# Kernel optimization log

Measured on AMD Instinct MI355X. Metric: run time of the kernel, lower is better.

Reference implementation:

```python
import jax, jax.numpy as jnp
import numpy as np

# class -> task group (from class_groups), and per-class distance thresholds
GROUP = jnp.array([0, 1, 1, 2, 2, 3, 4, 4, 5, 5], dtype=jnp.int32)
HIGH_T = jnp.array([2.0, 2.5, 2.5, 3.5, 2.5, 0.5, 1.0, 1.0, 0.5, 0.5], dtype=jnp.float32)
MED_T = jnp.array([4.0, 4.0, 4.0, 4.0, 4.0, 2.5, 2.5, 2.5, 2.0, 2.0], dtype=jnp.float32)
NEAR_THRESH = 30.0
FAR_THRESH = 50.0
FP_THRESH = 4.0


def setup_inputs() -> dict:
    key = jax.random.key(0)
    ks = jax.random.split(key, 7)
    B, R, G = 8, 4096, 512
    roi_xy = jax.random.uniform(ks[0], (B, R, 2), minval=-54.0, maxval=54.0)
    roi_rest = jax.random.normal(ks[1], (B, R, 7))
    rois = jnp.concatenate([roi_xy, roi_rest], axis=-1)            # (B,R,9)
    roi_scores = jax.random.uniform(ks[2], (B, R))                  # (B,R)
    roi_labels = jax.random.randint(ks[3], (B, R), 0, 10)           # (B,R)
    gt_xy = jax.random.uniform(ks[4], (B, G, 2), minval=-54.0, maxval=54.0)
    gt_rest = jax.random.normal(ks[5], (B, G, 7))
    gt_cls = jax.random.randint(ks[6], (B, G), 0, 10).astype(jnp.float32)
    gt_boxes_and_cls = jnp.concatenate([gt_xy, gt_rest, gt_cls[..., None]], axis=-1)  # (B,G,10)
    return {"rois": rois, "roi_scores": roi_scores, "gt_boxes_and_cls": gt_boxes_and_cls,
            "roi_labels": roi_labels, "batch_size": B}


def _forward(rois, roi_scores, gt, roi_labels):
    B, R, _ = rois.shape
    G = gt.shape[1]
    f32 = rois.dtype
    valid_roi = rois.sum(-1) != 0                                   # (B,R) padding filter
    valid_gt = gt.sum(-1) != 0                                      # (B,G)
    gt_cls = jnp.clip(gt[..., -1].astype(jnp.int32), 0, 9)         # (B,G)
    roi_grp = GROUP[jnp.clip(roi_labels.astype(jnp.int32), 0, 9)]  # (B,R)
    gt_grp = GROUP[gt_cls]                                          # (B,G)

    # BEV center distances (B,R,G) using x,y only
    diff = rois[:, :, None, :2] - gt[:, None, :, :2]
    d = jnp.sqrt((diff ** 2).sum(-1))

    same = roi_grp[:, :, None] == gt_grp[:, None, :]
    pv = valid_roi[:, :, None] & valid_gt[:, None, :]
    ht = HIGH_T[gt_cls][:, None, :]                                 # (B,1,G)->bcast
    mt = MED_T[gt_cls][:, None, :]
    high_mask = (d <= ht) & same & pv                               # (B,R,G)
    med_mask = (d > ht) & (d <= mt) & same & pv

    NEG = jnp.asarray(-1e9, f32)
    has_high = high_mask.any(axis=1)                                # (B,G)
    has_med = med_mask.any(axis=1)

    # best-scoring high ROI per GT
    hi = jnp.argmax(jnp.where(high_mask, roi_scores[:, :, None], NEG), axis=1)  # (B,G)
    high_roi = jnp.take_along_axis(rois, hi[:, :, None], axis=1)    # (B,G,9)
    high_score = jnp.take_along_axis(roi_scores, hi, axis=1)        # (B,G)
    refined_score = jnp.minimum((1.2 + high_score) / 2.0, 1.0)

    # best-scoring medium ROI per GT (used only when no high match)
    mi = jnp.argmax(jnp.where(med_mask, roi_scores[:, :, None], NEG), axis=1)
    med_roi = jnp.take_along_axis(rois, mi[:, :, None], axis=1)
    med_score = jnp.take_along_axis(roi_scores, mi, axis=1)
    sel_med = (~has_high) & has_med

    # unmatched GTs bucketed by range from ego (near/medium/far)
    unmatched = valid_gt & (~has_high) & (~has_med)
    rng = jnp.sqrt(gt[..., 0] ** 2 + gt[..., 1] ** 2)
    near = unmatched & (rng < NEAR_THRESH)
    far = unmatched & (rng > FAR_THRESH)
    midb = unmatched & (~near) & (~far)

    # false-positive ROIs: min distance to any valid GT > 4.0
    dmin = jnp.min(jnp.where(valid_gt[:, None, :], d, jnp.inf), axis=2)  # (B,R)
    fp = valid_roi & (dmin > FP_THRESH)

    hv = has_high.astype(f32)[..., None]
    mv = sel_med.astype(f32)[..., None]
    matched = (has_high | sel_med).astype(f32)[..., None]
    onehot = jnp.stack([near, midb, far], axis=-1).astype(f32)      # (B,G,3)
    outG = jnp.concatenate([
        high_roi * hv, (refined_score[..., None]) * hv, hv,
        med_roi * mv, (med_score[..., None]) * mv, mv,
        gt * matched, onehot], axis=-1)                             # (B,G,35)
    fpf = fp.astype(f32)
    outR = jnp.stack([fpf * roi_scores, fpf], axis=-1)              # (B,R,2)
    return jnp.concatenate([outG.reshape(B, -1), outR.reshape(B, -1)], axis=1)


def reference(rois, roi_scores, gt_boxes_and_cls, roi_labels, batch_size):
    return _forward(rois, roi_scores, gt_boxes_and_cls, roi_labels)
```

## Files before the change

### kernel.cpp

```cpp
#include <hip/hip_runtime.h>
#include <stdint.h>

#define NB 8
#define NR 4096
#define NG 512
#define OUTG 35
#define PER_B (NG*OUTG + NR*2)
#define GT_BLOCKS 512
#define FP_BLOCKS 128

__constant__ int   c_GROUP[10] = {0,1,1,2,2,3,4,4,5,5};
__constant__ float c_HIGH[10]  = {2.0f,2.5f,2.5f,3.5f,2.5f,0.5f,1.0f,1.0f,0.5f,0.5f};
__constant__ float c_MED[10]   = {4.0f,4.0f,4.0f,4.0f,4.0f,2.5f,2.5f,2.5f,2.0f,2.0f};

__device__ __forceinline__ float sqrt_le_bound(float t) {
  float B = t * t;
  while (sqrtf(__uint_as_float(__float_as_uint(B) + 1u)) <= t)
    B = __uint_as_float(__float_as_uint(B) + 1u);
  return B;
}

__global__ __launch_bounds__(256) void prep_kernel(
    const float* __restrict__ rois,
    const float* __restrict__ scores,
    const float* __restrict__ gt,
    const int*   __restrict__ labels,
    float4* __restrict__ ws_roi,
    float4* __restrict__ ws_gt) {
  int tid = blockIdx.x * 256 + threadIdx.x;
  if (tid < NB * NR) {
    const float* rr = rois + (size_t)tid * 9;
    float s = rr[0];
    #pragma unroll
    for (int k = 1; k < 9; ++k) s += rr[k];
    bool valid = (s != 0.0f);
    int lab = labels[tid];
    lab = min(max(lab, 0), 9);
    float w = valid ? (float)c_GROUP[lab] : -1.0f;
    ws_roi[tid] = make_float4(rr[0], rr[1], scores[tid], w);
  } else if (tid < NB * NR + NB * NG) {
    int i = tid - NB * NR;
    const float* gr = gt + (size_t)i * 10;
    float s = gr[0];
    #pragma unroll
    for (int k = 1; k < 10; ++k) s += gr[k];
    bool valid = (s != 0.0f);
    ws_gt[i] = make_float4(valid ? gr[0] : 1e30f, valid ? gr[1] : 1e30f, 0.f, 0.f);
  }
}

__device__ __forceinline__ void write_gt_row(
    float* __restrict__ og, const float gv[10], bool gvalid,
    unsigned long long uh, unsigned long long um,
    const float* __restrict__ rois_b) {
  bool has_high = (uh != 0ull);
  bool has_med  = (um != 0ull);
  bool sel_med  = (!has_high) && has_med;
  bool matched  = has_high || has_med;
  int   hi  = NR - 1 - (int)(unsigned int)(uh & 0xffffffffull);
  int   mi  = NR - 1 - (int)(unsigned int)(um & 0xffffffffull);
  float hsc = __uint_as_float((unsigned int)(uh >> 32) - 1u);
  float msc = __uint_as_float((unsigned int)(um >> 32) - 1u);
  const float* hr = rois_b + (size_t)(has_high ? hi : 0) * 9;
  const float* mr = rois_b + (size_t)(sel_med ? mi : 0) * 9;
  #pragma unroll
  for (int k = 0; k < 9; ++k) og[k] = has_high ? hr[k] : 0.0f;
  og[9]  = has_high ? fminf((1.2f + hsc) * 0.5f, 1.0f) : 0.0f;
  og[10] = has_high ? 1.0f : 0.0f;
  #pragma unroll
  for (int k = 0; k < 9; ++k) og[11 + k] = sel_med ? mr[k] : 0.0f;
  og[20] = sel_med ? msc : 0.0f;
  og[21] = sel_med ? 1.0f : 0.0f;
  #pragma unroll
  for (int k = 0; k < 10; ++k) og[22 + k] = matched ? gv[k] : 0.0f;
  bool unmatched = gvalid && !has_high && !has_med;
  float rng  = sqrtf(__fmul_rn(gv[0], gv[0]) + __fmul_rn(gv[1], gv[1]));
  bool nearb = unmatched && (rng < 30.0f);
  bool farb  = unmatched && (rng > 50.0f);
  bool midb  = unmatched && !nearb && !farb;
  og[32] = nearb ? 1.0f : 0.0f;
  og[33] = midb  ? 1.0f : 0.0f;
  og[34] = farb  ? 1.0f : 0.0f;
}

__global__ __launch_bounds__(256) void main_kernel(
    const float* __restrict__ rois,
    const float* __restrict__ gt,
    const float4* __restrict__ ws_roi,
    const float4* __restrict__ ws_gt,
    float* __restrict__ out) {
  __shared__ float2 sgt[NG];

  if (blockIdx.x < GT_BLOCKS) {
    int wave = threadIdx.x >> 6;
    int lane = threadIdx.x & 63;
    int widx = blockIdx.x * 4 + wave;
    int idx0 = widx * 2;
    int b    = idx0 >> 9;

    float gv0[10], gv1[10];
    {
      const float* g0 = gt + (size_t)idx0 * 10;
      #pragma unroll
      for (int k = 0; k < 10; ++k) gv0[k] = g0[k];
      #pragma unroll
      for (int k = 0; k < 10; ++k) gv1[k] = g0[10 + k];
    }
    float s0 = gv0[0], s1 = gv1[0];
    #pragma unroll
    for (int k = 1; k < 10; ++k) { s0 += gv0[k]; s1 += gv1[k]; }
    bool gvalid0 = (s0 != 0.0f), gvalid1 = (s1 != 0.0f);

    int cls0 = min(max((int)gv0[9], 0), 9);
    int cls1 = min(max((int)gv1[9], 0), 9);
    float Bh0 = sqrt_le_bound(c_HIGH[cls0]);
    float Bm0 = sqrt_le_bound(c_MED[cls0]);
    float Bh1 = sqrt_le_bound(c_HIGH[cls1]);
    float Bm1 = sqrt_le_bound(c_MED[cls1]);
    float gw0 = gvalid0 ? (float)c_GROUP[cls0] : -2.0f;
    float gw1 = gvalid1 ? (float)c_GROUP[cls1] : -2.0f;
    float gx0 = gv0[0], gy0 = gv0[1];
    float gx1 = gv1[0], gy1 = gv1[1];

    const float4* rp = ws_roi + (size_t)b * NR;
    unsigned long long uh0 = 0ull, um0 = 0ull, uh1 = 0ull, um1 = 0ull;
    #pragma unroll 4
    for (int r = lane; r < NR; r += 64) {
      float4 p = rp[r];
      unsigned long long key =
          ((unsigned long long)(__float_as_uint(p.z) + 1u) << 32) |
          (unsigned int)(NR - 1 - r);
      {
        float dx = p.x - gx0, dy = p.y - gy0;
        float d2 = __fmul_rn(dx, dx) + __fmul_rn(dy, dy);
        bool mm = (p.w == gw0) && (d2 <= Bm0);
        bool hh = mm && (d2 <= Bh0);
        bool ee = mm && !(d2 <= Bh0);
        if (hh && key > uh0) uh0 = key;
        if (ee && key > um0) um0 = key;
      }
      {
        float dx = p.x - gx1, dy = p.y - gy1;
        float d2 = __fmul_rn(dx, dx) + __fmul_rn(dy, dy);
        bool mm = (p.w == gw1) && (d2 <= Bm1);
        bool hh = mm && (d2 <= Bh1);
        bool ee = mm && !(d2 <= Bh1);
        if (hh && key > uh1) uh1 = key;
        if (ee && key > um1) um1 = key;
      }
    }
    #pragma unroll
    for (int off = 32; off > 0; off >>= 1) {
      unsigned long long t;
      t = __shfl_xor(uh0, off, 64); if (t > uh0) uh0 = t;
      t = __shfl_xor(um0, off, 64); if (t > um0) um0 = t;
      t = __shfl_xor(uh1, off, 64); if (t > uh1) uh1 = t;
      t = __shfl_xor(um1, off, 64); if (t > um1) um1 = t;
    }

    const float* rois_b = rois + (size_t)b * NR * 9;
    float* outb = out + (size_t)b * PER_B;
    if (lane == 0) {
      write_gt_row(outb + (size_t)(idx0 & 511) * OUTG, gv0, gvalid0, uh0, um0, rois_b);
    } else if (lane == 1) {
      write_gt_row(outb + (size_t)((idx0 + 1) & 511) * OUTG, gv1, gvalid1, uh1, um1, rois_b);
    }
  } else {
    int fb = blockIdx.x - GT_BLOCKS;
    int b  = fb >> 4;
    int r  = ((fb & 15) << 8) + threadIdx.x;

    const float4* gp = ws_gt + (size_t)b * NG;
    for (int j = threadIdx.x; j < NG; j += 256) {
      float4 v = gp[j];
      sgt[j] = make_float2(v.x, v.y);
    }
    __syncthreads();

    float4 p = ws_roi[(size_t)b * NR + r];
    float m2 = __builtin_inff();
    #pragma unroll 8
    for (int j = 0; j < NG; ++j) {
      float2 q = sgt[j];
      float dx = p.x - q.x, dy = p.y - q.y;
      float d2 = __fmul_rn(dx, dx) + __fmul_rn(dy, dy);
      m2 = fminf(m2, d2);
    }
    bool fp = (p.w >= 0.0f) && (sqrtf(m2) > 4.0f);
    float* orow = out + (size_t)b * PER_B + NG * OUTG + (size_t)r * 2;
    orow[0] = fp ? p.z : 0.0f;
    orow[1] = fp ? 1.0f : 0.0f;
  }
}

extern "C" void kernel_launch(void* const* d_in, const int* in_sizes, int n_in,
                              void* d_out, int out_size, void* d_ws, size_t ws_size,
                              hipStream_t stream) {
  const float* rois   = (const float*)d_in[0];
  const float* scores = (const float*)d_in[1];
  const float* gt     = (const float*)d_in[2];
  const int*   labels = (const int*)d_in[3];
  float* out = (float*)d_out;

  float4* ws_roi = (float4*)d_ws;
  float4* ws_gt  = ws_roi + (size_t)NB * NR;

  int total = NB * NR + NB * NG;
  prep_kernel<<<(total + 255) / 256, 256, 0, stream>>>(rois, scores, gt, labels,
                                                       ws_roi, ws_gt);
  main_kernel<<<GT_BLOCKS + FP_BLOCKS, 256, 0, stream>>>(rois, gt, ws_roi, ws_gt, out);
}
```

Before: 97.06 us.

## Fuse prep and main kernels, staging per-batch ROIs in shared memory

Removes the separate prep kernel and its workspace round trip. Each of 256 blocks (512 threads) now recomputes the packed ROI and GT records for its whole batch into shared memory (64KB of float4 plus 4KB), then does both the GT matching scan and a slice of the false-positive min-distance search. The FP search is split four ways per ROI with a shuffle reduction. This saves a launch and global traffic, at the cost of redundant per-batch prep work repeated 32 times per batch and lower occupancy from the large shared footprint.

```diff
diff --git a/kernel.cpp b/kernel.cpp
--- a/kernel.cpp
+++ b/kernel.cpp
@@ -6,8 +6,6 @@
 #define NG 512
 #define OUTG 35
 #define PER_B (NG*OUTG + NR*2)
-#define GT_BLOCKS 512
-#define FP_BLOCKS 128
 
 __constant__ int   c_GROUP[10] = {0,1,1,2,2,3,4,4,5,5};
 __constant__ float c_HIGH[10]  = {2.0f,2.5f,2.5f,3.5f,2.5f,0.5f,1.0f,1.0f,0.5f,0.5f};
@@ -18,35 +16,6 @@
   while (sqrtf(__uint_as_float(__float_as_uint(B) + 1u)) <= t)
     B = __uint_as_float(__float_as_uint(B) + 1u);
   return B;
-}
-
-__global__ __launch_bounds__(256) void prep_kernel(
-    const float* __restrict__ rois,
-    const float* __restrict__ scores,
-    const float* __restrict__ gt,
-    const int*   __restrict__ labels,
-    float4* __restrict__ ws_roi,
-    float4* __restrict__ ws_gt) {
-  int tid = blockIdx.x * 256 + threadIdx.x;
-  if (tid < NB * NR) {
-    const float* rr = rois + (size_t)tid * 9;
-    float s = rr[0];
-    #pragma unroll
-    for (int k = 1; k < 9; ++k) s += rr[k];
-    bool valid = (s != 0.0f);
-    int lab = labels[tid];
-    lab = min(max(lab, 0), 9);
-    float w = valid ? (float)c_GROUP[lab] : -1.0f;
-    ws_roi[tid] = make_float4(rr[0], rr[1], scores[tid], w);
-  } else if (tid < NB * NR + NB * NG) {
-    int i = tid - NB * NR;
-    const float* gr = gt + (size_t)i * 10;
-    float s = gr[0];
-    #pragma unroll
-    for (int k = 1; k < 10; ++k) s += gr[k];
-    bool valid = (s != 0.0f);
-    ws_gt[i] = make_float4(valid ? gr[0] : 1e30f, valid ? gr[1] : 1e30f, 0.f, 0.f);
-  }
 }
 
 __device__ __forceinline__ void write_gt_row(
@@ -83,113 +52,140 @@
   og[34] = farb  ? 1.0f : 0.0f;
 }
 
-__global__ __launch_bounds__(256) void main_kernel(
+__global__ __launch_bounds__(512) void fused_kernel(
     const float* __restrict__ rois,
+    const float* __restrict__ scores,
     const float* __restrict__ gt,
-    const float4* __restrict__ ws_roi,
-    const float4* __restrict__ ws_gt,
+    const int*   __restrict__ labels,
     float* __restrict__ out) {
+  __shared__ float4 sroi[NR];
   __shared__ float2 sgt[NG];
 
-  if (blockIdx.x < GT_BLOCKS) {
-    int wave = threadIdx.x >> 6;
-    int lane = threadIdx.x & 63;
-    int widx = blockIdx.x * 4 + wave;
-    int idx0 = widx * 2;
-    int b    = idx0 >> 9;
-
-    float gv0[10], gv1[10];
+  int tid = threadIdx.x;
+  int bid = blockIdx.x;
+  int b   = bid >> 5;
+  int sub = bid & 31;
+
+  const float* rois_b = rois   + (size_t)b * NR * 9;
+  const float* sc_b   = scores + (size_t)b * NR;
+  const int*   lab_b  = labels + (size_t)b * NR;
+  const float* gt_b   = gt     + (size_t)b * NG * 10;
+
+  #pragma unroll 4
+  for (int k = 0; k < 8; ++k) {
+    int r = tid + k * 512;
+    const float* rr = rois_b + (size_t)r * 9;
+    float s = rr[0];
+    #pragma unroll
+    for (int j = 1; j < 9; ++j) s += rr[j];
+    bool valid = (s != 0.0f);
+    int lab = min(max(lab_b[r], 0), 9);
+    float w = valid ? (float)c_GROUP[lab] : -1.0f;
+    sroi[r] = make_float4(rr[0], rr[1], sc_b[r], w);
+  }
+  {
+    const float* gr = gt_b + (size_t)tid * 10;
+    float s = gr[0];
+    #pragma unroll
+    for (int j = 1; j < 10; ++j) s += gr[j];
+    bool valid = (s != 0.0f);
+    sgt[tid] = make_float2(valid ? gr[0] : 1e30f, valid ? gr[1] : 1e30f);
+  }
+  __syncthreads();
+
+  int wave = tid >> 6;
+  int lane = tid & 63;
+  int g0   = sub * 16 + wave * 2;
+
+  float gv0[10], gv1[10];
+  {
+    const float* gp = gt_b + (size_t)g0 * 10;
+    #pragma unroll
+    for (int k = 0; k < 10; ++k) gv0[k] = gp[k];
+    #pragma unroll
+    for (int k = 0; k < 10; ++k) gv1[k] = gp[10 + k];
+  }
+  float s0 = gv0[0], s1 = gv1[0];
+  #pragma unroll
+  for (int k = 1; k < 10; ++k) { s0 += gv0[k]; s1 += gv1[k]; }
+  bool gvalid0 = (s0 != 0.0f), gvalid1 = (s1 != 0.0f);
+
+  int cls0 = min(max((int)gv0[9], 0), 9);
+  int cls1 = min(max((int)gv1[9], 0), 9);
+  float Bh0 = sqrt_le_bound(c_HIGH[cls0]);
+  float Bm0 = sqrt_le_bound(c_MED[cls0]);
+  float Bh1 = sqrt_le_bound(c_HIGH[cls1]);
+  float Bm1 = sqrt_le_bound(c_MED[cls1]);
+  float gw0 = gvalid0 ? (float)c_GROUP[cls0] : -2.0f;
+  float gw1 = gvalid1 ? (float)c_GROUP[cls1] : -2.0f;
+  float gx0 = gv0[0], gy0 = gv0[1];
+  float gx1 = gv1[0], gy1 = gv1[1];
+
+  unsigned long long uh0 = 0ull, um0 = 0ull, uh1 = 0ull, um1 = 0ull;
+  #pragma unroll 4
+  for (int r = lane; r < NR; r += 64) {
+    float4 p = sroi[r];
+    unsigned long long key =
+        ((unsigned long long)(__float_as_uint(p.z) + 1u) << 32) |
+        (unsigned int)(NR - 1 - r);
     {
-      const float* g0 = gt + (size_t)idx0 * 10;
-      #pragma unroll
-      for (int k = 0; k < 10; ++k) gv0[k] = g0[k];
-      #pragma unroll
-      for (int k = 0; k < 10; ++k) gv1[k] = g0[10 + k];
-    }
-    float s0 = gv0[0], s1 = gv1[0];
-    #pragma unroll
-    for (int k = 1; k < 10; ++k) { s0 += gv0[k]; s1 += gv1[k]; }
-    bool gvalid0 = (s0 != 0.0f), gvalid1 = (s1 != 0.0f);
-
-    int cls0 = min(max((int)gv0[9], 0), 9);
-    int cls1 = min(max((int)gv1[9], 0), 9);
-    float Bh0 = sqrt_le_bound(c_HIGH[cls0]);
-    float Bm0 = sqrt_le_bound(c_MED[cls0]);
-    float Bh1 = sqrt_le_bound(c_HIGH[cls1]);
-    float Bm1 = sqrt_le_bound(c_MED[cls1]);
-    float gw0 = gvalid0 ? (float)c_GROUP[cls0] : -2.0f;
-    float gw1 = gvalid1 ? (float)c_GROUP[cls1] : -2.0f;
-    float gx0 = gv0[0], gy0 = gv0[1];
-    float gx1 = gv1[0], gy1 = gv1[1];
-
-    const float4* rp = ws_roi + (size_t)b * NR;
-    unsigned long long uh0 = 0ull, um0 = 0ull, uh1 = 0ull, um1 = 0ull;
+      float dx = p.x - gx0, dy = p.y - gy0;
+      float d2 = __fmul_rn(dx, dx) + __fmul_rn(dy, dy);
+      bool mm = (p.w == gw0) && (d2 <= Bm0);
+      bool hh = mm && (d2 <= Bh0);
+      bool ee = mm && !(d2 <= Bh0);
+      if (hh && key > uh0) uh0 = key;
+      if (ee && key > um0) um0 = key;
+    }
+    {
+      float dx = p.x - gx1, dy = p.y - gy1;
+      float d2 = __fmul_rn(dx, dx) + __fmul_rn(dy, dy);
+      bool mm = (p.w == gw1) && (d2 <= Bm1);
+      bool hh = mm && (d2 <= Bh1);
+      bool ee = mm && !(d2 <= Bh1);
+      if (hh && key > uh1) uh1 = key;
+      if (ee && key > um1) um1 = key;
+    }
+  }
+  #pragma unroll
+  for (int off = 32; off > 0; off >>= 1) {
+    unsigned long long t;
+    t = __shfl_xor(uh0, off, 64); if (t > uh0) uh0 = t;
+    t = __shfl_xor(um0, off, 64); if (t > um0) um0 = t;
+    t = __shfl_xor(uh1, off, 64); if (t > uh1) uh1 = t;
+    t = __shfl_xor(um1, off, 64); if (t > um1) um1 = t;
+  }
+
+  float* outb = out + (size_t)b * PER_B;
+  if (lane == 0) {
+    write_gt_row(outb + (size_t)g0 * OUTG, gv0, gvalid0, uh0, um0, rois_b);
+  } else if (lane == 1) {
+    write_gt_row(outb + (size_t)(g0 + 1) * OUTG, gv1, gvalid1, uh1, um1, rois_b);
+  }
+
+  {
+    int rl = tid >> 2;
+    int q  = tid & 3;
+    int r  = sub * 128 + rl;
+    float4 p = sroi[r];
+    float m2 = __builtin_inff();
     #pragma unroll 4
-    for (int r = lane; r < NR; r += 64) {
-      float4 p = rp[r];
-      unsigned long long key =
-          ((unsigned long long)(__float_as_uint(p.z) + 1u) << 32) |
-          (unsigned int)(NR - 1 - r);
-      {
-        float dx = p.x - gx0, dy = p.y - gy0;
-        float d2 = __fmul_rn(dx, dx) + __fmul_rn(dy, dy);
-        bool mm = (p.w == gw0) && (d2 <= Bm0);
-        bool hh = mm && (d2 <= Bh0);
-        bool ee = mm && !(d2 <= Bh0);
-        if (hh && key > uh0) uh0 = key;
-        if (ee && key > um0) um0 = key;
-      }
-      {
-        float dx = p.x - gx1, dy = p.y - gy1;
-        float d2 = __fmul_rn(dx, dx) + __fmul_rn(dy, dy);
-        bool mm = (p.w == gw1) && (d2 <= Bm1);
-        bool hh = mm && (d2 <= Bh1);
-        bool ee = mm && !(d2 <= Bh1);
-        if (hh && key > uh1) uh1 = key;
-        if (ee && key > um1) um1 = key;
-      }
-    }
-    #pragma unroll
-    for (int off = 32; off > 0; off >>= 1) {
-      unsigned long long t;
-      t = __shfl_xor(uh0, off, 64); if (t > uh0) uh0 = t;
-      t = __shfl_xor(um0, off, 64); if (t > um0) um0 = t;
-      t = __shfl_xor(uh1, off, 64); if (t > uh1) uh1 = t;
-      t = __shfl_xor(um1, off, 64); if (t > um1) um1 = t;
-    }
-
-    const float* rois_b = rois + (size_t)b * NR * 9;
-    float* outb = out + (size_t)b * PER_B;
-    if (lane == 0) {
-      write_gt_row(outb + (size_t)(idx0 & 511) * OUTG, gv0, gvalid0, uh0, um0, rois_b);
-    } else if (lane == 1) {
-      write_gt_row(outb + (size_t)((idx0 + 1) & 511) * OUTG, gv1, gvalid1, uh1, um1, rois_b);
-    }
-  } else {
-    int fb = blockIdx.x - GT_BLOCKS;
-    int b  = fb >> 4;
-    int r  = ((fb & 15) << 8) + threadIdx.x;
-
-    const float4* gp = ws_gt + (size_t)b * NG;
-    for (int j = threadIdx.x; j < NG; j += 256) {
-      float4 v = gp[j];
-      sgt[j] = make_float2(v.x, v.y);
-    }
-    __syncthreads();
-
-    float4 p = ws_roi[(size_t)b * NR + r];
-    float m2 = __builtin_inff();
-    #pragma unroll 8
-    for (int j = 0; j < NG; ++j) {
-      float2 q = sgt[j];
-      float dx = p.x - q.x, dy = p.y - q.y;
+    for (int jj = 0; jj < 128; ++jj) {
+      int j = q * 128 + ((jj + q * 4) & 127);
+      float2 qq = sgt[j];
+      float dx = p.x - qq.x, dy = p.y - qq.y;
       float d2 = __fmul_rn(dx, dx) + __fmul_rn(dy, dy);
       m2 = fminf(m2, d2);
     }
-    bool fp = (p.w >= 0.0f) && (sqrtf(m2) > 4.0f);
-    float* orow = out + (size_t)b * PER_B + NG * OUTG + (size_t)r * 2;
-    orow[0] = fp ? p.z : 0.0f;
-    orow[1] = fp ? 1.0f : 0.0f;
+    float t;
+    t = __shfl_xor(m2, 1, 64); m2 = fminf(m2, t);
+    t = __shfl_xor(m2, 2, 64); m2 = fminf(m2, t);
+    if (q == 0) {
+      bool fp = (p.w >= 0.0f) && (sqrtf(m2) > 4.0f);
+      float* orow = out + (size_t)b * PER_B + NG * OUTG + (size_t)r * 2;
+      orow[0] = fp ? p.z : 0.0f;
+      orow[1] = fp ? 1.0f : 0.0f;
+    }
   }
 }
 
@@ -201,12 +197,7 @@
   const float* gt     = (const float*)d_in[2];
   const int*   labels = (const int*)d_in[3];
   float* out = (float*)d_out;
-
-  float4* ws_roi = (float4*)d_ws;
-  float4* ws_gt  = ws_roi + (size_t)NB * NR;
-
-  int total = NB * NR + NB * NG;
-  prep_kernel<<<(total + 255) / 256, 256, 0, stream>>>(rois, scores, gt, labels,
-                                                       ws_roi, ws_gt);
-  main_kernel<<<GT_BLOCKS + FP_BLOCKS, 256, 0, stream>>>(rois, gt, ws_roi, ws_gt, out);
-}
+  (void)d_ws; (void)ws_size;
+
+  fused_kernel<<<NB * 32, 512, 0, stream>>>(rois, scores, gt, labels, out);
+}
```

Result: faster. 92.68 us (-4.5%).
